# Kernel optimization log

Measured on AMD Instinct MI355X. Metric: run time of the kernel, lower is better.

The kernel has to match this reference:

```python
import jax, jax.numpy as jnp
import numpy as np

H, W = 16, 16  # input_resolution
NUM_HEADS = 16
DIM = 512


def build_relative_position_index(h, w):
    coords = np.stack(np.meshgrid(np.arange(h), np.arange(w), indexing='ij'))  # [2,h,w]
    cf = coords.reshape(2, -1)
    rel = cf[:, :, None] - cf[:, None, :]            # [2,N,N]
    rel = rel.transpose(1, 2, 0).astype(np.int32)    # [N,N,2]
    rel[:, :, 0] += h - 1
    rel[:, :, 1] += w - 1
    rel[:, :, 0] *= 2 * w - 1
    return jnp.asarray(rel.sum(-1).reshape(-1), dtype=jnp.int32)  # [N*N]


def setup_inputs() -> dict:
    key = jax.random.key(0)
    ks = jax.random.split(key, 6)
    B, N, C = 128, H * W, DIM
    x = jax.random.normal(ks[0], (B, N, C), dtype=jnp.float32)
    qkv_w = jax.random.normal(ks[1], (3 * C, C), dtype=jnp.float32) * (C ** -0.5)
    qkv_b = jax.random.normal(ks[2], (3 * C,), dtype=jnp.float32) * 0.02
    proj_w = jax.random.normal(ks[3], (C, C), dtype=jnp.float32) * (C ** -0.5)
    proj_b = jax.random.normal(ks[4], (C,), dtype=jnp.float32) * 0.02
    bias_table = jax.random.normal(ks[5], ((2 * H - 1) * (2 * W - 1), NUM_HEADS), dtype=jnp.float32) * 0.02
    rel_index = build_relative_position_index(H, W)
    return {"x": x, "qkv_w": qkv_w, "qkv_b": qkv_b, "proj_w": proj_w,
            "proj_b": proj_b, "bias_table": bias_table, "rel_index": rel_index}


def reference(x, qkv_w, qkv_b, proj_w, proj_b, bias_table, rel_index):
    B, N, C = x.shape
    h = NUM_HEADS
    hd = C // h
    scale = hd ** -0.5
    # qkv projection: [B,N,3C] -> [3,B,h,N,hd]
    qkv = (jnp.einsum('bnc,oc->bno', x, qkv_w) + qkv_b)
    qkv = qkv.reshape(B, N, 3, h, hd).transpose(2, 0, 3, 1, 4)
    q, k, v = qkv[0], qkv[1], qkv[2]
    # relative position bias: gather [N*N,h] -> [1,h,N,N]
    bias = bias_table[rel_index].reshape(N, N, h).transpose(2, 0, 1)[None]
    attn = jnp.einsum('bhnd,bhmd->bhnm', q * scale, k) + bias
    attn = jax.nn.softmax(attn, axis=-1)
    out = jnp.einsum('bhnm,bhmd->bhnd', attn, v)     # [B,h,N,hd]
    out = out.transpose(0, 2, 1, 3).reshape(B, N, C)
    return jnp.einsum('bnc,oc->bno', out, proj_w) + proj_b
```

## Files before the change

### kernel.cpp

```cpp
#include <hip/hip_runtime.h>

typedef __bf16 bf16_t;
typedef __bf16 bf16x8 __attribute__((ext_vector_type(8)));
typedef float f32x4 __attribute__((ext_vector_type(4)));

#define MFMA_16x16x32(a, b, c) __builtin_amdgcn_mfma_f32_16x16x32_bf16((a), (b), (c), 0, 0, 0)

__device__ inline bf16x8 cvt8(const float* __restrict__ p) {
  bf16x8 r;
#pragma unroll
  for (int j = 0; j < 8; j++) r[j] = (bf16_t)p[j];
  return r;
}

__device__ inline void load_lds16(const bf16_t* g, bf16_t* l) {
  __builtin_amdgcn_global_load_lds(
      (const __attribute__((address_space(1))) void*)g,
      (__attribute__((address_space(3))) void*)l, 16, 0, 0);
}

__global__ __launch_bounds__(256) void convert_k(
    const float* __restrict__ x, const float* __restrict__ qkv_w,
    const float* __restrict__ proj_w,
    bf16_t* __restrict__ xbf, bf16_t* __restrict__ wqkvbf,
    bf16_t* __restrict__ wprojbf) {
  size_t base = ((size_t)blockIdx.x * 256 + threadIdx.x) * 8;
  if (base < 16777216) {
    *(bf16x8*)(xbf + base) = cvt8(x + base);
  } else if (base < 17563648) {
    size_t o = base - 16777216;
    *(bf16x8*)(wqkvbf + o) = cvt8(qkv_w + o);
  } else {
    size_t o = base - 17563648;
    *(bf16x8*)(wprojbf + o) = cvt8(proj_w + o);
  }
}

__global__ __launch_bounds__(256) void bias_gather_k(
    const float* __restrict__ table, const int* __restrict__ rel,
    float* __restrict__ biasws) {
  int idx = blockIdx.x * 256 + threadIdx.x;
  int h = idx >> 16;
  int rem = idx & 65535;
  int rb = rem >> 12;
  int ct = (rem >> 8) & 15;
  int L = (rem >> 2) & 63;
  int r = idx & 3;
  int row = rb * 16 + (L >> 4) * 4 + r;
  int col = ct * 16 + (L & 15);
  biasws[idx] = table[rel[row * 256 + col] * 16 + h];
}

#define PH_MID()                                          \
  do {                                                    \
    __builtin_amdgcn_s_barrier();                         \
    asm volatile("s_waitcnt lgkmcnt(0)" ::: "memory");    \
    __builtin_amdgcn_sched_barrier(0);                    \
    __builtin_amdgcn_s_setprio(1);                        \
  } while (0)

#define PH_END()                                          \
  do {                                                    \
    __buil_noop();                                        \
  } while (0)

__device__ __forceinline__ void __builtin_dummy() {}
#undef PH_END
#define PH_END()                                          \
  do {                                                    \
    __builtin_amdgcn_s_setprio(0);                        \
    __builtin_amdgcn_s_barrier();                         \
    __builtin_amdgcn_sched_barrier(0);                    \
  } while (0)

#define STGA(buf, tl, c)                                                         \
  do {                                                                           \
    load_lds16(ga + (size_t)(tl)*64 + (c)*32768, la + (buf)*16384 + (c)*4096);   \
    load_lds16(ga + (size_t)(tl)*64 + ((c) + 1) * 32768,                         \
               la + (buf)*16384 + ((c) + 1) * 4096);                             \
  } while (0)
#define STGB(buf, tl, c)                                                         \
  do {                                                                           \
    load_lds16(gb + (size_t)(tl)*64 + (c)*32768, lb + (buf)*16384 + (c)*4096);   \
    load_lds16(gb + (size_t)(tl)*64 + ((c) + 1) * 32768,                         \
               lb + (buf)*16384 + ((c) + 1) * 4096);                             \
  } while (0)

#define RDA(dst, buf, ibase)                                                     \
  _Pragma("unroll") for (int i = 0; i < 4; ++i) {                                \
    dst[i][0] = *(const bf16x8*)&As[(buf)*16384 + a0 + ((ibase) + i) * 1024];    \
    dst[i][1] = *(const bf16x8*)&As[(buf)*16384 + a1 + ((ibase) + i) * 1024];    \
  }
#define RDB(dst, buf, jbase)                                                     \
  _Pragma("unroll") for (int j = 0; j < 2; ++j) {                                \
    dst[j][0] = *(const bf16x8*)&Bs[(buf)*16384 + b0 + ((jbase) + j) * 1024];    \
    dst[j][1] = *(const bf16x8*)&Bs[(buf)*16384 + b1 + ((jbase) + j) * 1024];    \
  }

#define MFQ(Af, Bf, I0, J0)                                                      \
  _Pragma("unroll") for (int i = 0; i < 4; ++i) _Pragma("unroll")                \
      for (int j = 0; j < 2; ++j) {                                              \
    acc[(I0) + i][(J0) + j] =                                                    \
        MFMA_16x16x32(Af[i][0], Bf[j][0], acc[(I0) + i][(J0) + j]);              \
    acc[(I0) + i][(J0) + j] =                                                    \
        MFMA_16x16x32(Af[i][1], Bf[j][1], acc[(I0) + i][(J0) + j]);              \
  }

__device__ __forceinline__ void gemm256_core(
    const bf16_t* __restrict__ Ap, const bf16_t* __restrict__ Wp,
    int m0, int n0, f32x4 (&acc)[8][4]) {
  __shared__ bf16_t As[2 * 16384];
  __shared__ bf16_t Bs[2 * 16384];
  const int t = threadIdx.x;
  const int w = t >> 6, L = t & 63;
  const int wm = w >> 2, wn = w & 3;
  const int lrow = L & 15, lq = L >> 4;

  const int srow = t >> 3;
  const int sslot = (t & 7) ^ (srow & 7);
  const bf16_t* ga = Ap + (size_t)(m0 + srow) * 512 + sslot * 8;
  const bf16_t* gb = Wp + (size_t)(n0 + srow) * 512 + sslot * 8;
  bf16_t* la = As + t * 8;
  bf16_t* lb = Bs + t * 8;

  const int m8 = (lrow & 7) * 8;
  const int a0 = (wm * 128 + lrow) * 64 + ((lq * 8) ^ m8);
  const int a1 = (wm * 128 + lrow) * 64 + ((32 + lq * 8) ^ m8);
  const int b0 = (wn * 64 + lrow) * 64 + ((lq * 8) ^ m8);
  const int b1 = (wn * 64 + lrow) * 64 + ((32 + lq * 8) ^ m8);

  STGA(0, 0, 0); STGA(0, 0, 2); STGB(0, 0, 0); STGB(0, 0, 2);
  STGA(1, 1, 0); STGA(1, 1, 2); STGB(1, 1, 0); STGB(1, 1, 2);
  asm volatile("s_waitcnt vmcnt(8)" ::: "memory");
  __builtin_amdgcn_s_barrier();
  __builtin_amdgcn_sched_barrier(0);

#pragma unroll
  for (int it = 0; it < 4; ++it) {
    {
      bf16x8 fal[4][2], fah[4][2], fbl[2][2], fbh[2][2];
      RDA(fal, 0, 0); RDB(fbl, 0, 0);
      if (it > 0) STGB(1, 2 * it + 1, 0);
      PH_MID(); MFQ(fal, fbl, 0, 0); PH_END();
      RDA(fah, 0, 4); RDB(fbh, 0, 2);
      if (it > 0) STGB(1, 2 * it + 1, 2);
      PH_MID(); MFQ(fah, fbh, 4, 2); PH_END();
      if (it < 3) STGA(0, 2 * it + 2, 0);
      PH_MID(); MFQ(fal, fbh, 0, 2); PH_END();
      if (it < 3) STGA(0, 2 * it + 2, 2);
      PH_MID(); MFQ(fah, fbl, 4, 0);
      __builtin_amdgcn_s_setprio(0);
      if (it < 3) asm volatile("s_waitcnt vmcnt(4)" ::: "memory");
      else        asm volatile("s_waitcnt vmcnt(0)" ::: "memory");
      __builtin_amdgcn_s_barrier();
      __builtin_amdgcn_sched_barrier(0);
    }
    {
      bf16x8 fal[4][2], fah[4][2], fbl[2][2], fbh[2][2];
      RDA(fal, 1, 0); RDB(fbl, 1, 0);
      if (it < 3) STGB(0, 2 * it + 2, 0);
      PH_MID(); MFQ(fal, fbl, 0, 0); PH_END();
      RDA(fah, 1, 4); RDB(fbh, 1, 2);
      if (it < 3) STGB(0, 2 * it + 2, 2);
      PH_MID(); MFQ(fah, fbh, 4, 2); PH_END();
      if (it < 3) STGA(1, 2 * it + 3, 0);
      PH_MID(); MFQ(fal, fbh, 0, 2); PH_END();
      if (it < 3) STGA(1, 2 * it + 3, 2);
      PH_MID(); MFQ(fah, fbl, 4, 0);
      __builtin_amdgcn_s_setprio(0);
      if (it < 3) {
        asm volatile("s_waitcnt vmcnt(4)" ::: "memory");
        __builtin_amdgcn_s_barrier();
        __builtin_amdgcn_sched_barrier(0);
      }
    }
  }
}

__global__ __launch_bounds__(512, 2) void qkv_gemm256_k(
    const bf16_t* __restrict__ A, const bf16_t* __restrict__ W,
    const float* __restrict__ Bvec,
    bf16_t* __restrict__ qws, bf16_t* __restrict__ kws, bf16_t* __restrict__ vws) {
  const int id = blockIdx.x;
  const int wg = (id & 7) * 96 + (id >> 3);
  const int mt = wg / 6, nt = wg % 6;
  const int m0 = mt * 256, n0 = nt * 256;

  f32x4 acc[8][4] = {};
  gemm256_core(A, W, m0, n0, acc);

  const int t = threadIdx.x;
  const int w = t >> 6, L = t & 63;
  const int wm = w >> 2, wn = w & 3;
  const int lrow = L & 15, lq = L >> 4;
  const int col0 = n0 + wn * 64;
  const int s = col0 >> 9;
  bf16_t* dst = (s == 0) ? qws : (s == 1) ? kws : vws;
  const float mul = (s == 0) ? 0.17677669529663687f : 1.0f;
#pragma unroll
  for (int jj = 0; jj < 4; ++jj) {
    int o = col0 + jj * 16 + lrow;
    float bias = Bvec[o];
    int rem = o & 511;
    int hh = rem >> 5, d = rem & 31;
#pragma unroll
    for (int i = 0; i < 8; ++i) {
#pragma unroll
      for (int r = 0; r < 4; ++r) {
        int m = m0 + wm * 128 + i * 16 + lq * 4 + r;
        int b = m >> 8, n = m & 255;
        dst[(size_t)(((b * 16 + hh) * 256 + n) << 5) + d] =
            (bf16_t)((acc[i][jj][r] + bias) * mul);
      }
    }
  }
}

__global__ __launch_bounds__(512, 2) void proj_gemm256_k(
    const bf16_t* __restrict__ A, const bf16_t* __restrict__ W,
    const float* __restrict__ Bvec, float* __restrict__ out) {
  const int id = blockIdx.x;
  const int wg = (id & 7) * 32 + (id >> 3);
  const int mt = wg >> 1, nt = wg & 1;
  const int m0 = mt * 256, n0 = nt * 256;

  f32x4 acc[8][4] = {};
  gemm256_core(A, W, m0, n0, acc);

  const int t = threadIdx.x;
  const int w = t >> 6, L = t & 63;
  const int wm = w >> 2, wn = w & 3;
  const int lrow = L & 15, lq = L >> 4;
#pragma unroll
  for (int jj = 0; jj < 4; ++jj) {
    int o = n0 + wn * 64 + jj * 16 + lrow;
    float bias = Bvec[o];
#pragma unroll
    for (int i = 0; i < 8; ++i) {
#pragma unroll
      for (int r = 0; r < 4; ++r) {
        int m = m0 + wm * 128 + i * 16 + lq * 4 + r;
        out[(size_t)m * 512 + o] = acc[i][jj][r] + bias;
      }
    }
  }
}

__global__ __launch_bounds__(256) void attn_k(
    const bf16_t* __restrict__ qws, const bf16_t* __restrict__ kws,
    const bf16_t* __restrict__ vws, const float* __restrict__ biasws,
    bf16_t* __restrict__ aows) {
  __shared__ __align__(16) char smem[33792 + 16896];
  bf16_t* Ps = (bf16_t*)smem;
  bf16_t* Vs = (bf16_t*)(smem + 33792);

  const int id = blockIdx.x;
  const int xcd = id & 7;
  const int jj = id >> 3;
  const int bh = (jj >> 2) * 8 + xcd;
  const int strip = jj & 3;
  const int h = bh & 15, b = bh >> 4;

  const int t = threadIdx.x;
  const int w = t >> 6, L = t & 63;
  const int lrow = L & 15, lq = L >> 4;

  const bf16_t* kbase = kws + (size_t)bh * 8192;
  const bf16_t* vbase = vws + (size_t)bh * 8192;
#pragma unroll
  for (int c = 0; c < 4; c++) {
    bf16x8 vv = *(const bf16x8*)(vbase + t * 32 + c * 8);
#pragma unroll
    for (int j = 0; j < 8; j++) Vs[(c * 8 + j) * 264 + t] = vv[j];
  }

  const bf16_t* qbase = qws + (size_t)bh * 8192 + (strip * 64 + w * 16) * 32;
  bf16x8 qf = *(const bf16x8*)(qbase + lrow * 32 + lq * 8);
  bf16x8 kf[16];
#pragma unroll
  for (int ct = 0; ct < 16; ct++)
    kf[ct] = *(const bf16x8*)(kbase + (ct * 16 + lrow) * 32 + lq * 8);

  const float* bb = biasws + h * 65536 + (strip * 4 + w) * 4096;
  f32x4 S[16];
#pragma unroll
  for (int ct = 0; ct < 16; ct++) {
    f32x4 bi = *(const f32x4*)(bb + ct * 256 + L * 4);
    S[ct] = MFMA_16x16x32(qf, kf[ct], bi);
  }

  float sm[4] = {0.f, 0.f, 0.f, 0.f};
#pragma unroll
  for (int ct = 0; ct < 16; ct++)
#pragma unroll
    for (int r = 0; r < 4; r++) {
      float e = __expf(S[ct][r]);
      S[ct][r] = e;
      sm[r] += e;
    }
#pragma unroll
  for (int r = 0; r < 4; r++)
#pragma unroll
    for (int msk = 1; msk < 16; msk <<= 1)
      sm[r] += __shfl_xor(sm[r], msk, 64);
  float inv[4];
#pragma unroll
  for (int r = 0; r < 4; r++) inv[r] = 1.0f / sm[r];

  bf16_t* Pw = Ps + w * 4224;
#pragma unroll
  for (int ct = 0; ct < 16; ct++)
#pragma unroll
    for (int r = 0; r < 4; r++)
      Pw[(lq * 4 + r) * 264 + ct * 16 + lrow] = (bf16_t)S[ct][r];

  __syncthreads();

  f32x4 O0 = {}, O1 = {};
#pragma unroll
  for (int c = 0; c < 8; c++) {
    bf16x8 pf = *(const bf16x8*)&Pw[lrow * 264 + c * 32 + lq * 8];
    bf16x8 v0 = *(const bf16x8*)&Vs[lrow * 264 + c * 32 + lq * 8];
    bf16x8 v1 = *(const bf16x8*)&Vs[(16 + lrow) * 264 + c * 32 + lq * 8];
    O0 = MFMA_16x16x32(pf, v0, O0);
    O1 = MFMA_16x16x32(pf, v1, O1);
  }
  bf16_t* obase = aows + (size_t)(b * 256 + strip * 64 + w * 16) * 512 + h * 32;
#pragma unroll
  for (int r = 0; r < 4; r++) {
    int rl = lq * 4 + r;
    obase[rl * 512 + lrow] = (bf16_t)(O0[r] * inv[r]);
    obase[rl * 512 + 16 + lrow] = (bf16_t)(O1[r] * inv[r]);
  }
}

extern "C" void kernel_launch(void* const* d_in, const int* in_sizes, int n_in,
                              void* d_out, int out_size, void* d_ws, size_t ws_size,
                              hipStream_t stream) {
  (void)in_sizes; (void)n_in; (void)out_size; (void)ws_size;
  const float* x      = (const float*)d_in[0];
  const float* qkv_w  = (const float*)d_in[1];
  const float* qkv_b  = (const float*)d_in[2];
  const float* proj_w = (const float*)d_in[3];
  const float* proj_b = (const float*)d_in[4];
  const float* table  = (const float*)d_in[5];
  const int*   rel    = (const int*)d_in[6];

  const size_t QKV_ELEMS = 16777216;
  bf16_t* qws     = (bf16_t*)d_ws;
  bf16_t* kws     = qws + QKV_ELEMS;
  bf16_t* vws     = kws + QKV_ELEMS;
  float*  biasws  = (float*)(vws + QKV_ELEMS);
  bf16_t* wqkvbf  = (bf16_t*)(biasws + 1048576);
  bf16_t* wprojbf = wqkvbf + 786432;
  bf16_t* xbf     = wprojbf + 262144;
  bf16_t* aows    = xbf;
  float*  out     = (float*)d_out;

  convert_k<<<8704, 256, 0, stream>>>(x, qkv_w, proj_w, xbf, wqkvbf, wprojbf);
  bias_gather_k<<<4096, 256, 0, stream>>>(table, rel, biasws);
  qkv_gemm256_k<<<768, 512, 0, stream>>>(xbf, wqkvbf, qkv_b, qws, kws, vws);
  attn_k<<<8192, 256, 0, stream>>>(qws, kws, vws, biasws, aows);
  proj_gemm256_k<<<256, 512, 0, stream>>>(aows, wprojbf, proj_b, out);
}
```

Before: 292.7 us.

## Make QKV GEMM persistent over three N tiles with continuous A-reusing pipeline

The QKV GEMM launches 256 workgroups instead of 768. Each workgroup keeps its 256-row A slab and walks three output N tiles in one continuous software pipeline of 24 K-steps, storing each finished tile mid-stream. Bias is preloaded into the accumulators instead of being added in the epilogue, and the MFMA/LDS read order within each phase is reshuffled. This aims to remove per-tile prologue and drain bubbles and improve A reuse. The cost is fewer workgroups on 256 CUs (one per CU), which lowers occupancy and leaves the epilogue stores serialized inside the main loop.

```diff
diff --git a/kernel.cpp b/kernel.cpp
--- a/kernel.cpp
+++ b/kernel.cpp
@@ -61,28 +61,22 @@
 
 #define PH_END()                                          \
   do {                                                    \
-    __buil_noop();                                        \
-  } while (0)
-
-__device__ __forceinline__ void __builtin_dummy() {}
-#undef PH_END
-#define PH_END()                                          \
-  do {                                                    \
     __builtin_amdgcn_s_setprio(0);                        \
     __builtin_amdgcn_s_barrier();                         \
     __builtin_amdgcn_sched_barrier(0);                    \
   } while (0)
 
-#define STGA(buf, tl, c)                                                         \
+#define STG_A2(buf, g, c)                                                        \
   do {                                                                           \
-    load_lds16(ga + (size_t)(tl)*64 + (c)*32768, la + (buf)*16384 + (c)*4096);   \
-    load_lds16(ga + (size_t)(tl)*64 + ((c) + 1) * 32768,                         \
+    load_lds16(ga + ((g)&7) * 64 + (c)*32768, la + (buf)*16384 + (c)*4096);      \
+    load_lds16(ga + ((g)&7) * 64 + ((c) + 1) * 32768,                            \
                la + (buf)*16384 + ((c) + 1) * 4096);                             \
   } while (0)
-#define STGB(buf, tl, c)                                                         \
+#define STG_B2(buf, g, c)                                                        \
   do {                                                                           \
-    load_lds16(gb + (size_t)(tl)*64 + (c)*32768, lb + (buf)*16384 + (c)*4096);   \
-    load_lds16(gb + (size_t)(tl)*64 + ((c) + 1) * 32768,                         \
+    load_lds16(gb + ((g) >> 3) * 131072 + ((g)&7) * 64 + (c)*32768,              \
+               lb + (buf)*16384 + (c)*4096);                                     \
+    load_lds16(gb + ((g) >> 3) * 131072 + ((g)&7) * 64 + ((c) + 1) * 32768,      \
                lb + (buf)*16384 + ((c) + 1) * 4096);                             \
   } while (0)
 
@@ -106,111 +100,144 @@
         MFMA_16x16x32(Af[i][1], Bf[j][1], acc[(I0) + i][(J0) + j]);              \
   }
 
-__device__ __forceinline__ void gemm256_core(
-    const bf16_t* __restrict__ Ap, const bf16_t* __restrict__ Wp,
-    int m0, int n0, f32x4 (&acc)[8][4]) {
-  __shared__ bf16_t As[2 * 16384];
-  __shared__ bf16_t Bs[2 * 16384];
-  const int t = threadIdx.x;
-  const int w = t >> 6, L = t & 63;
-  const int wm = w >> 2, wn = w & 3;
-  const int lrow = L & 15, lq = L >> 4;
-
-  const int srow = t >> 3;
-  const int sslot = (t & 7) ^ (srow & 7);
-  const bf16_t* ga = Ap + (size_t)(m0 + srow) * 512 + sslot * 8;
-  const bf16_t* gb = Wp + (size_t)(n0 + srow) * 512 + sslot * 8;
-  bf16_t* la = As + t * 8;
-  bf16_t* lb = Bs + t * 8;
-
-  const int m8 = (lrow & 7) * 8;
-  const int a0 = (wm * 128 + lrow) * 64 + ((lq * 8) ^ m8);
-  const int a1 = (wm * 128 + lrow) * 64 + ((32 + lq * 8) ^ m8);
-  const int b0 = (wn * 64 + lrow) * 64 + ((lq * 8) ^ m8);
+#define GROUP(G, NT)                                                             \
+  do {                                                                           \
+    {                                                                            \
+      bf16x8 fal[4][2], fbl[2][2], fah[4][2], fbh[2][2];                         \
+      RDA(fal, 0, 0); RDB(fbl, 0, 0);                                            \
+      if ((2 * (G) + 1) < (NT)) STG_B2(1, 2 * (G) + 1, 0);                       \
+      PH_MID(); MFQ(fal, fbl, 0, 0); PH_END();                                   \
+      RDA(fah, 0, 4);                                                            \
+      if ((2 * (G) + 1) < (NT)) STG_B2(1, 2 * (G) + 1, 2);                       \
+      PH_MID(); MFQ(fah, fbl, 4, 0); PH_END();                                   \
+      RDB(fbh, 0, 2);                                                            \
+      if ((2 * (G) + 2) < (NT)) STG_A2(0, 2 * (G) + 2, 0);                       \
+      PH_MID(); MFQ(fah, fbh, 4, 2); PH_END();                                   \
+      if ((2 * (G) + 2) < (NT)) STG_A2(0, 2 * (G) + 2, 2);                       \
+      PH_MID(); MFQ(fal, fbh, 0, 2);                                             \
+      __builtin_amdgcn_s_setprio(0);                                             \
+      if ((2 * (G) + 2) < (NT))                                                  \
+        asm volatile("s_waitcnt vmcnt(4)" ::: "memory");                         \
+      else                                                                       \
+        asm volatile("s_waitcnt vmcnt(0)" ::: "memory");                         \
+      __builtin_amdgcn_s_barrier();                                              \
+      __builtin_amdgcn_sched_barrier(0);                                         \
+    }                                                                            \
+    {                                                                            \
+      bf16x8 fal[4][2], fbl[2][2], fah[4][2], fbh[2][2];                         \
+      RDA(fal, 1, 0); RDB(fbl, 1, 0);                                            \
+      if ((2 * (G) + 2) < (NT)) STG_B2(0, 2 * (G) + 2, 0);                       \
+      PH_MID(); MFQ(fal, fbl, 0, 0); PH_END();                                   \
+      RDA(fah, 1, 4);                                                            \
+      if ((2 * (G) + 2) < (NT)) STG_B2(0, 2 * (G) + 2, 2);                       \
+      PH_MID(); MFQ(fah, fbl, 4, 0); PH_END();                                   \
+      RDB(fbh, 1, 2);                                                            \
+      if ((2 * (G) + 3) < (NT)) STG_A2(1, 2 * (G) + 3, 0);                       \
+      PH_MID(); MFQ(fah, fbh, 4, 2); PH_END();                                   \
+      if ((2 * (G) + 3) < (NT)) STG_A2(1, 2 * (G) + 3, 2);                       \
+      PH_MID(); MFQ(fal, fbh, 0, 2);                                             \
+      __builtin_amdgcn_s_setprio(0);                                             \
+      if ((2 * (G) + 3) < (NT))                                                  \
+        asm volatile("s_waitcnt vmcnt(4)" ::: "memory");                         \
+      else                                                                       \
+        asm volatile("s_waitcnt vmcnt(0)" ::: "memory");                         \
+      __builtin_amdgcn_s_barrier();                                              \
+      __builtin_amdgcn_sched_barrier(0);                                         \
+    }                                                                            \
+  } while (0)
+
+#define GEMM_SETUP(Ap, Wp)                                                       \
+  __shared__ bf16_t As[2 * 16384];                                               \
+  __shared__ bf16_t Bs[2 * 16384];                                               \
+  const int t = threadIdx.x;                                                     \
+  const int w = t >> 6, L = t & 63;                                              \
+  const int wm = w >> 2, wn = w & 3;                                             \
+  const int lrow = L & 15, lq = L >> 4;                                          \
+  const int srow = t >> 3;                                                       \
+  const int sslot = (t & 7) ^ (srow & 7);                                        \
+  const bf16_t* ga = (Ap) + (size_t)(m0 + srow) * 512 + sslot * 8;               \
+  const bf16_t* gb = (Wp) + (size_t)(n0 + srow) * 512 + sslot * 8;               \
+  bf16_t* la = As + t * 8;                                                       \
+  bf16_t* lb = Bs + t * 8;                                                       \
+  const int m8 = (lrow & 7) * 8;                                                 \
+  const int a0 = (wm * 128 + lrow) * 64 + ((lq * 8) ^ m8);                       \
+  const int a1 = (wm * 128 + lrow) * 64 + ((32 + lq * 8) ^ m8);                  \
+  const int b0 = (wn * 64 + lrow) * 64 + ((lq * 8) ^ m8);                        \
   const int b1 = (wn * 64 + lrow) * 64 + ((32 + lq * 8) ^ m8);
 
-  STGA(0, 0, 0); STGA(0, 0, 2); STGB(0, 0, 0); STGB(0, 0, 2);
-  STGA(1, 1, 0); STGA(1, 1, 2); STGB(1, 1, 0); STGB(1, 1, 2);
-  asm volatile("s_waitcnt vmcnt(8)" ::: "memory");
-  __builtin_amdgcn_s_barrier();
+#define PROLOGUE()                                                               \
+  STG_A2(0, 0, 0); STG_A2(0, 0, 2);                                              \
+  STG_B2(0, 0, 0); STG_B2(0, 0, 2);                                              \
+  STG_A2(1, 1, 0); STG_A2(1, 1, 2);                                              \
+  asm volatile("s_waitcnt vmcnt(4)" ::: "memory");                               \
+  __builtin_amdgcn_s_barrier();                                                  \
   __builtin_amdgcn_sched_barrier(0);
-
-#pragma unroll
-  for (int it = 0; it < 4; ++it) {
-    {
-      bf16x8 fal[4][2], fah[4][2], fbl[2][2], fbh[2][2];
-      RDA(fal, 0, 0); RDB(fbl, 0, 0);
-      if (it > 0) STGB(1, 2 * it + 1, 0);
-      PH_MID(); MFQ(fal, fbl, 0, 0); PH_END();
-      RDA(fah, 0, 4); RDB(fbh, 0, 2);
-      if (it > 0) STGB(1, 2 * it + 1, 2);
-      PH_MID(); MFQ(fah, fbh, 4, 2); PH_END();
-      if (it < 3) STGA(0, 2 * it + 2, 0);
-      PH_MID(); MFQ(fal, fbh, 0, 2); PH_END();
-      if (it < 3) STGA(0, 2 * it + 2, 2);
-      PH_MID(); MFQ(fah, fbl, 4, 0);
-      __builtin_amdgcn_s_setprio(0);
-      if (it < 3) asm volatile("s_waitcnt vmcnt(4)" ::: "memory");
-      else        asm volatile("s_waitcnt vmcnt(0)" ::: "memory");
-      __builtin_amdgcn_s_barrier();
-      __builtin_amdgcn_sched_barrier(0);
-    }
-    {
-      bf16x8 fal[4][2], fah[4][2], fbl[2][2], fbh[2][2];
-      RDA(fal, 1, 0); RDB(fbl, 1, 0);
-      if (it < 3) STGB(0, 2 * it + 2, 0);
-      PH_MID(); MFQ(fal, fbl, 0, 0); PH_END();
-      RDA(fah, 1, 4); RDB(fbh, 1, 2);
-      if (it < 3) STGB(0, 2 * it + 2, 2);
-      PH_MID(); MFQ(fah, fbh, 4, 2); PH_END();
-      if (it < 3) STGA(1, 2 * it + 3, 0);
-      PH_MID(); MFQ(fal, fbh, 0, 2); PH_END();
-      if (it < 3) STGA(1, 2 * it + 3, 2);
-      PH_MID(); MFQ(fah, fbl, 4, 0);
-      __builtin_amdgcn_s_setprio(0);
-      if (it < 3) {
-        asm volatile("s_waitcnt vmcnt(4)" ::: "memory");
-        __builtin_amdgcn_s_barrier();
-        __builtin_amdgcn_sched_barrier(0);
-      }
-    }
-  }
-}
 
 __global__ __launch_bounds__(512, 2) void qkv_gemm256_k(
     const bf16_t* __restrict__ A, const bf16_t* __restrict__ W,
     const float* __restrict__ Bvec,
     bf16_t* __restrict__ qws, bf16_t* __restrict__ kws, bf16_t* __restrict__ vws) {
   const int id = blockIdx.x;
-  const int wg = (id & 7) * 96 + (id >> 3);
-  const int mt = wg / 6, nt = wg % 6;
-  const int m0 = mt * 256, n0 = nt * 256;
-
-  f32x4 acc[8][4] = {};
-  gemm256_core(A, W, m0, n0, acc);
-
-  const int t = threadIdx.x;
-  const int w = t >> 6, L = t & 63;
-  const int wm = w >> 2, wn = w & 3;
-  const int lrow = L & 15, lq = L >> 4;
-  const int col0 = n0 + wn * 64;
-  const int s = col0 >> 9;
-  bf16_t* dst = (s == 0) ? qws : (s == 1) ? kws : vws;
-  const float mul = (s == 0) ? 0.17677669529663687f : 1.0f;
-#pragma unroll
-  for (int jj = 0; jj < 4; ++jj) {
-    int o = col0 + jj * 16 + lrow;
-    float bias = Bvec[o];
-    int rem = o & 511;
-    int hh = rem >> 5, d = rem & 31;
-#pragma unroll
-    for (int i = 0; i < 8; ++i) {
-#pragma unroll
-      for (int r = 0; r < 4; ++r) {
-        int m = m0 + wm * 128 + i * 16 + lq * 4 + r;
-        int b = m >> 8, n = m & 255;
-        dst[(size_t)(((b * 16 + hh) * 256 + n) << 5) + d] =
-            (bf16_t)((acc[i][jj][r] + bias) * mul);
+  const int lin = (id & 7) * 32 + (id >> 3);
+  const int mt = lin >> 1;
+  const int ntb = (lin & 1) * 3;
+  const int m0 = mt * 256;
+  const int n0 = ntb * 256;
+
+  GEMM_SETUP(A, W);
+
+  float bias_r[3][4];
+#pragma unroll
+  for (int ot = 0; ot < 3; ++ot) {
+    int c0 = (ntb + ot) * 256 + wn * 64;
+#pragma unroll
+    for (int jj = 0; jj < 4; ++jj) bias_r[ot][jj] = Bvec[c0 + jj * 16 + lrow];
+  }
+
+  f32x4 acc[8][4];
+#pragma unroll
+  for (int i = 0; i < 8; ++i)
+#pragma unroll
+    for (int jj = 0; jj < 4; ++jj) {
+      float bv = bias_r[0][jj];
+      acc[i][jj] = (f32x4){bv, bv, bv, bv};
+    }
+
+  PROLOGUE();
+
+#pragma unroll
+  for (int G = 0; G < 12; ++G) {
+    GROUP(G, 24);
+    if ((G & 3) == 3) {
+      const int ot = G >> 2;
+      const int col0 = (ntb + ot) * 256 + wn * 64;
+      const int s = col0 >> 9;
+      bf16_t* dst = (s == 0) ? qws : (s == 1) ? kws : vws;
+      const float mul = (s == 0) ? 0.17677669529663687f : 1.0f;
+#pragma unroll
+      for (int jj = 0; jj < 4; ++jj) {
+        int o = col0 + jj * 16 + lrow;
+        int rem = o & 511;
+        int hh = rem >> 5, d = rem & 31;
+#pragma unroll
+        for (int i = 0; i < 8; ++i) {
+#pragma unroll
+          for (int r = 0; r < 4; ++r) {
+            int m = m0 + wm * 128 + i * 16 + lq * 4 + r;
+            int b = m >> 8, n = m & 255;
+            dst[(size_t)(((b * 16 + hh) * 256 + n) << 5) + d] =
+                (bf16_t)(acc[i][jj][r] * mul);
+          }
+        }
+      }
+      if (ot < 2) {
+#pragma unroll
+        for (int i = 0; i < 8; ++i)
+#pragma unroll
+          for (int jj = 0; jj < 4; ++jj) {
+            float bv = bias_r[ot + 1][jj];
+            acc[i][jj] = (f32x4){bv, bv, bv, bv};
+          }
       }
     }
   }
@@ -220,27 +247,40 @@
     const bf16_t* __restrict__ A, const bf16_t* __restrict__ W,
     const float* __restrict__ Bvec, float* __restrict__ out) {
   const int id = blockIdx.x;
-  const int wg = (id & 7) * 32 + (id >> 3);
-  const int mt = wg >> 1, nt = wg & 1;
+  const int lin = (id & 7) * 32 + (id >> 3);
+  const int mt = lin >> 1, nt = lin & 1;
   const int m0 = mt * 256, n0 = nt * 256;
 
-  f32x4 acc[8][4] = {};
-  gemm256_core(A, W, m0, n0, acc);
-
-  const int t = threadIdx.x;
-  const int w = t >> 6, L = t & 63;
-  const int wm = w >> 2, wn = w & 3;
-  const int lrow = L & 15, lq = L >> 4;
+  GEMM_SETUP(A, W);
+
+  float bias_r[4];
+#pragma unroll
+  for (int jj = 0; jj < 4; ++jj)
+    bias_r[jj] = Bvec[n0 + wn * 64 + jj * 16 + lrow];
+
+  f32x4 acc[8][4];
+#pragma unroll
+  for (int i = 0; i < 8; ++i)
+#pragma unroll
+    for (int jj = 0; jj < 4; ++jj) {
+      float bv = bias_r[jj];
+      acc[i][jj] = (f32x4){bv, bv, bv, bv};
+    }
+
+  PROLOGUE();
+
+#pragma unroll
+  for (int G = 0; G < 4; ++G) GROUP(G, 8);
+
 #pragma unroll
   for (int jj = 0; jj < 4; ++jj) {
     int o = n0 + wn * 64 + jj * 16 + lrow;
-    float bias = Bvec[o];
 #pragma unroll
     for (int i = 0; i < 8; ++i) {
 #pragma unroll
       for (int r = 0; r < 4; ++r) {
         int m = m0 + wm * 128 + i * 16 + lq * 4 + r;
-        out[(size_t)m * 512 + o] = acc[i][jj][r] + bias;
+        out[(size_t)m * 512 + o] = acc[i][jj][r];
       }
     }
   }
@@ -359,7 +399,7 @@
 
   convert_k<<<8704, 256, 0, stream>>>(x, qkv_w, proj_w, xbf, wqkvbf, wprojbf);
   bias_gather_k<<<4096, 256, 0, stream>>>(table, rel, biasws);
-  qkv_gemm256_k<<<768, 512, 0, stream>>>(xbf, wqkvbf, qkv_b, qws, kws, vws);
+  qkv_gemm256_k<<<256, 512, 0, stream>>>(xbf, wqkvbf, qkv_b, qws, kws, vws);
   attn_k<<<8192, 256, 0, stream>>>(qws, kws, vws, biasws, aows);
   proj_gemm256_k<<<256, 512, 0, stream>>>(aows, wprojbf, proj_b, out);
 }
```

After: 314.1 us. 1.07x slower.
